# Kernel tuning notes

Measured on AMD Instinct MI355X. Metric: run time of the kernel, lower is better.

## Reference

```python
import jax, jax.numpy as jnp
import numpy as np

T, B, I, H = 512, 64, 512, 512

def setup_inputs() -> dict:
    key = jax.random.key(0)
    ks = jax.random.split(key, 16)
    s_i = 1.0 / np.sqrt(I)
    s_h = 1.0 / np.sqrt(H)
    return {
        "input": jax.random.normal(ks[0], (T, B, I), jnp.float32),
        "hidden": jax.random.normal(ks[1], (B, H), jnp.float32),
        "zt_w_w": jax.random.uniform(ks[2], (1, I), jnp.float32, -s_i, s_i),
        "zt_w_b": jax.random.uniform(ks[3], (1,), jnp.float32, -s_i, s_i),
        "zt_u_w": jax.random.uniform(ks[4], (1, H), jnp.float32, -s_h, s_h),
        "zt_u_b": jax.random.uniform(ks[5], (1,), jnp.float32, -s_h, s_h),
        "rt_w_w": jax.random.uniform(ks[6], (1, I), jnp.float32, -s_i, s_i),
        "rt_w_b": jax.random.uniform(ks[7], (1,), jnp.float32, -s_i, s_i),
        "rt_u_w": jax.random.uniform(ks[8], (1, H), jnp.float32, -s_h, s_h),
        "rt_u_b": jax.random.uniform(ks[9], (1,), jnp.float32, -s_h, s_h),
        "h_w_w": jax.random.uniform(ks[10], (H, I), jnp.float32, -s_i, s_i),
        "h_w_b": jax.random.uniform(ks[11], (H,), jnp.float32, -s_i, s_i),
        "h_u_w": jax.random.uniform(ks[12], (H, H), jnp.float32, -s_h, s_h),
        "h_u_b": jax.random.uniform(ks[13], (H,), jnp.float32, -s_h, s_h),
    }

def reference(input, hidden, zt_w_w, zt_w_b, zt_u_w, zt_u_b,
              rt_w_w, rt_w_b, rt_u_w, rt_u_b, h_w_w, h_w_b, h_u_w, h_u_b):
    # Input-dependent projections are h-independent: precompute over all T.
    xz = jnp.einsum('tbi,oi->tbo', input, zt_w_w) + zt_w_b  # [T,B,1]
    xr = jnp.einsum('tbi,oi->tbo', input, rt_w_w) + rt_w_b  # [T,B,1]
    xn = jnp.einsum('tbi,hi->tbh', input, h_w_w) + h_w_b    # [T,B,H]

    def step(h, xs):
        xz_t, xr_t, xn_t = xs
        zt = jax.nn.sigmoid(xz_t + h @ zt_u_w.T + zt_u_b)   # [B,1]
        rt = jax.nn.sigmoid(xr_t + h @ rt_u_w.T + rt_u_b)   # [B,1]
        # NOTE: faithful to source: h_u(hidden) * rt (gate applied AFTER linear)
        nt = jnp.tanh(xn_t + (h @ h_u_w.T + h_u_b) * rt)    # [B,H]
        h_new = (1.0 - zt) * nt + zt * h
        return h_new, h_new

    hidden_final, output = jax.lax.scan(step, hidden, (xz, xr, xn))
    return output, hidden_final
```

## Files before the change

### kernel.cpp

```cpp
#include <hip/hip_runtime.h>
#include <hip/hip_fp16.h>

#define T_DIM 512
#define B_DIM 64
#define I_DIM 512
#define H_DIM 512
#define BH (B_DIM * H_DIM)
#define TBH ((size_t)T_DIM * BH)

typedef __attribute__((ext_vector_type(8))) short short8;
typedef __attribute__((ext_vector_type(4))) float f32x4;

#define SW16(r, k) ((r) * 512 + ((k) ^ (((r) & 15) << 3)))

__device__ __forceinline__ unsigned short f2bf(float x) {
    unsigned int u = __float_as_uint(x);
    u = u + 0x7FFFu + ((u >> 16) & 1u);
    return (unsigned short)(u >> 16);
}
__device__ __forceinline__ float bf2f(unsigned short s) {
    return __uint_as_float(((unsigned int)s) << 16);
}
__device__ __forceinline__ float uasf(unsigned int u) { return __uint_as_float(u); }

__device__ __forceinline__ void ld128_coh(uint4& d, const void* p) {
    asm volatile("global_load_dwordx4 %0, %1, off sc0 sc1"
                 : "=v"(d) : "v"(p) : "memory");
}
__device__ __forceinline__ void ld128_coh_wait(uint4& d, const void* p) {
    asm volatile("global_load_dwordx4 %0, %1, off sc0 sc1\n\t"
                 "s_waitcnt vmcnt(0)"
                 : "=v"(d) : "v"(p) : "memory");
}
__device__ __forceinline__ void ld32f(float& d, const void* p) {
    asm volatile("global_load_dword %0, %1, off" : "=v"(d) : "v"(p));
}
__device__ __forceinline__ void ld32u(unsigned int& d, const void* p) {
    asm volatile("global_load_dword %0, %1, off" : "=v"(d) : "v"(p));
}

__global__ __launch_bounds__(256) void xzr_kernel(
    const float* __restrict__ input,
    const float* __restrict__ zw, const float* __restrict__ zb,
    const float* __restrict__ rw, const float* __restrict__ rb,
    unsigned int* __restrict__ xzr, unsigned int* __restrict__ flags)
{
    const int tid = threadIdx.x, bx = blockIdx.x;
    if (bx == 0 && tid < 32) flags[tid] = 0u;
    const int row = bx * 4 + (tid >> 6);
    const int lane = tid & 63;
    const float* p = input + (size_t)row * I_DIM + lane * 8;
    float x[8], z[8], r[8];
    *(float4*)(x)     = *(const float4*)(p);
    *(float4*)(x + 4) = *(const float4*)(p + 4);
    *(float4*)(z)     = *(const float4*)(zw + lane * 8);
    *(float4*)(z + 4) = *(const float4*)(zw + lane * 8 + 4);
    *(float4*)(r)     = *(const float4*)(rw + lane * 8);
    *(float4*)(r + 4) = *(const float4*)(rw + lane * 8 + 4);
    float pz = 0.f, pr = 0.f;
#pragma unroll
    for (int i = 0; i < 8; i++) { pz += x[i] * z[i]; pr += x[i] * r[i]; }
#pragma unroll
    for (int off = 32; off > 0; off >>= 1) {
        pz += __shfl_xor(pz, off);
        pr += __shfl_xor(pr, off);
    }
    if (lane == 0) {
        unsigned int uz = __half_as_ushort(__float2half(pz + zb[0]));
        unsigned int ur = __half_as_ushort(__float2half(pr + rb[0]));
        xzr[row] = (uz << 16) | ur;
    }
}

#define APITCH 40

__global__ __launch_bounds__(256, 2) void xn_gemm_kernel(
    const float* __restrict__ A, const float* __restrict__ W,
    const float* __restrict__ bias, float* __restrict__ C)
{
    __shared__ __align__(16) unsigned short a_hi[64 * APITCH], a_lo[64 * APITCH];
    __shared__ __align__(16) unsigned short b_hi[64 * APITCH], b_lo[64 * APITCH];
    const int tid = threadIdx.x;
    const int bx = blockIdx.x;
    const int mt = bx >> 3, ntile = bx & 7;
    const int wv = tid >> 6, lane = tid & 63;
    const int srow = tid >> 2, skseg = (tid & 3) * 8;
    const int m = lane & 15;
    const int ko = (lane >> 4) * 8;

    f32x4 ahh[4], ahl[4], alh[4];
#pragma unroll
    for (int i = 0; i < 4; i++) { ahh[i] = (f32x4)0.f; ahl[i] = (f32x4)0.f; alh[i] = (f32x4)0.f; }

    for (int kt = 0; kt < 16; ++kt) {
        {
            float fa[8], fb[8];
            const float* pa = A + (size_t)(mt * 64 + srow) * I_DIM + kt * 32 + skseg;
            *(float4*)(fa)     = *(const float4*)(pa);
            *(float4*)(fa + 4) = *(const float4*)(pa + 4);
            const float* pb = W + (size_t)(ntile * 64 + srow) * I_DIM + kt * 32 + skseg;
            *(float4*)(fb)     = *(const float4*)(pb);
            *(float4*)(fb + 4) = *(const float4*)(pb + 4);
            short8 hi, lo;
#pragma unroll
            for (int i = 0; i < 8; i++) {
                unsigned short h = f2bf(fa[i]);
                hi[i] = (short)h; lo[i] = (short)f2bf(fa[i] - bf2f(h));
            }
            *(short8*)&a_hi[srow * APITCH + skseg] = hi;
            *(short8*)&a_lo[srow * APITCH + skseg] = lo;
#pragma unroll
            for (int i = 0; i < 8; i++) {
                unsigned short h = f2bf(fb[i]);
                hi[i] = (short)h; lo[i] = (short)f2bf(fb[i] - bf2f(h));
            }
            *(short8*)&b_hi[srow * APITCH + skseg] = hi;
            *(short8*)&b_lo[srow * APITCH + skseg] = lo;
        }
        __syncthreads();
        short8 vah = *(const short8*)&a_hi[(wv * 16 + m) * APITCH + ko];
        short8 val = *(const short8*)&a_lo[(wv * 16 + m) * APITCH + ko];
#pragma unroll
        for (int ns = 0; ns < 4; ++ns) {
            short8 vbh = *(const short8*)&b_hi[(ns * 16 + m) * APITCH + ko];
            short8 vbl = *(const short8*)&b_lo[(ns * 16 + m) * APITCH + ko];
            ahh[ns] = __builtin_amdgcn_mfma_f32_16x16x32_bf16(vah, vbh, ahh[ns], 0, 0, 0);
            ahl[ns] = __builtin_amdgcn_mfma_f32_16x16x32_bf16(vah, vbl, ahl[ns], 0, 0, 0);
            alh[ns] = __builtin_amdgcn_mfma_f32_16x16x32_bf16(val, vbh, alh[ns], 0, 0, 0);
        }
        __syncthreads();
    }
#pragma unroll
    for (int ns = 0; ns < 4; ++ns) {
#pragma unroll
        for (int rr = 0; rr < 4; ++rr) {
            int rowd = wv * 16 + (lane >> 4) * 4 + rr;
            int cold = ntile * 64 + ns * 16 + (lane & 15);
            float v = ahh[ns][rr] + ahl[ns][rr] + alh[ns][rr] + bias[cold];
            C[(size_t)(mt * 64 + rowd) * H_DIM + cold] = v;
        }
    }
}

__global__ __launch_bounds__(256, 1) void rnn_kernel(
    const float* __restrict__ h0,
    const unsigned int* __restrict__ xzr,
    const float* __restrict__ zuw, const float* __restrict__ ruw,
    const float* __restrict__ zub, const float* __restrict__ rub,
    const float* __restrict__ huw, const float* __restrict__ hub,
    float* __restrict__ out,
    char* __restrict__ xbuf, unsigned int* __restrict__ flags)
{
    __shared__ __align__(16) unsigned short hs_hi[16 * 512], hs_lo[16 * 512];
    __shared__ float zu[512], ru[512];
    __shared__ float zg[16], rg[16];

    const int tid = threadIdx.x;
    const int bid = blockIdx.x;
    const int g = bid >> 3, js = bid & 7;
    const int wv = tid >> 6, lane = tid & 63;
    const int quad = lane >> 4, am = lane & 15;
    const int col = js * 64 + wv * 16 + am;
    const int ko = quad * 8;
    const int gr = tid >> 4, gs = tid & 15;

    for (int i = tid; i < 512; i += 256) { zu[i] = zuw[i]; ru[i] = ruw[i]; }
    const float zbias = zub[0], rbias = rub[0];
    const float hubl = hub[col];

    short8 wh[16], wl[16];
#pragma unroll
    for (int kt = 0; kt < 16; ++kt) {
        float f[8];
        const float* p = huw + (size_t)col * H_DIM + kt * 32 + ko;
        *(float4*)(f)     = *(const float4*)(p);
        *(float4*)(f + 4) = *(const float4*)(p + 4);
#pragma unroll
        for (int i = 0; i < 8; i++) {
            unsigned short h = f2bf(f[i]);
            wh[kt][i] = (short)h;
            wl[kt][i] = (short)f2bf(f[i] - bf2f(h));
        }
    }

#pragma unroll
    for (int i = 0; i < 8; i++) {
        int idx = tid * 4 + i * 1024;
        int row = idx >> 9, k = idx & 511;
        float4 f = *(const float4*)(h0 + (size_t)(g * 16 + row) * H_DIM + k);
        float fa[4] = {f.x, f.y, f.z, f.w};
        unsigned int h_[4], l_[4];
#pragma unroll
        for (int j = 0; j < 4; j++) {
            h_[j] = f2bf(fa[j]);
            l_[j] = f2bf(fa[j] - bf2f((unsigned short)h_[j]));
        }
        int a = SW16(row, k);
        uint2 hv = { h_[0] | (h_[1] << 16), h_[2] | (h_[3] << 16) };
        uint2 lv = { l_[0] | (l_[1] << 16), l_[2] | (l_[3] << 16) };
        *(uint2*)&hs_hi[a] = hv;
        *(uint2*)&hs_lo[a] = lv;
    }
    float hkeep[4];
#pragma unroll
    for (int rr = 0; rr < 4; ++rr)
        hkeep[rr] = h0[(size_t)(g * 16 + quad * 4 + rr) * H_DIM + col];
    __syncthreads();

    float xnv0, xnv1, xnv2, xnv3;
    unsigned int zrw;
#define PREFETCH(tt) do {                                                     \
        const float* xp_ = out + (size_t)(tt) * BH +                          \
                           (size_t)(g * 16 + quad * 4) * H_DIM + col;         \
        ld32f(xnv0, xp_);        ld32f(xnv1, xp_ + H_DIM);                    \
        ld32f(xnv2, xp_ + 2 * H_DIM); ld32f(xnv3, xp_ + 3 * H_DIM);           \
        ld32u(zrw, xzr + (tt) * B_DIM + g * 16 + gr);                         \
    } while (0)
    PREFETCH(0);

    for (int t = 0; t < T_DIM; ++t) {
        asm volatile("s_waitcnt vmcnt(0)"
                     : "+v"(xnv0), "+v"(xnv1), "+v"(xnv2), "+v"(xnv3), "+v"(zrw)
                     :: "memory");
        float pz = 0.f, pr = 0.f;
#pragma unroll
        for (int i = 0; i < 8; i++) {
            int k = gs * 4 + i * 64;
            int a = SW16(gr, k);
            uint2 hw = *(const uint2*)&hs_hi[a];
            uint2 lw = *(const uint2*)&hs_lo[a];
            float4 zv = *(const float4*)&zu[k];
            float4 rv = *(const float4*)&ru[k];
            float h0f = uasf(hw.x << 16) + uasf(lw.x << 16);
            float h1f = uasf(hw.x & 0xFFFF0000u) + uasf(lw.x & 0xFFFF0000u);
            float h2f = uasf(hw.y << 16) + uasf(lw.y << 16);
            float h3f = uasf(hw.y & 0xFFFF0000u) + uasf(lw.y & 0xFFFF0000u);
            pz += h0f * zv.x + h1f * zv.y + h2f * zv.z + h3f * zv.w;
            pr += h0f * rv.x + h1f * rv.y + h2f * rv.z + h3f * rv.w;
        }
#pragma unroll
        for (int off = 8; off > 0; off >>= 1) {
            pz += __shfl_xor(pz, off);
            pr += __shfl_xor(pr, off);
        }
        if (gs == 0) {
            float xzf = __half2float(__ushort_as_half((unsigned short)(zrw >> 16)));
            float xrf = __half2float(__ushort_as_half((unsigned short)(zrw & 0xFFFFu)));
            zg[gr] = 1.f / (1.f + __expf(-(xzf + pz + zbias)));
            rg[gr] = 1.f / (1.f + __expf(-(xrf + pr + rbias)));
        }
        __syncthreads();

        f32x4 hh = (f32x4)0.f, hl = (f32x4)0.f, lh = (f32x4)0.f;
#pragma unroll
        for (int kt = 0; kt < 16; ++kt) {
            short8 ah = *(const short8*)&hs_hi[SW16(am, kt * 32 + ko)];
            short8 al = *(const short8*)&hs_lo[SW16(am, kt * 32 + ko)];
            hh = __builtin_amdgcn_mfma_f32_16x16x32_bf16(ah, wh[kt], hh, 0, 0, 0);
            hl = __builtin_amdgcn_mfma_f32_16x16x32_bf16(ah, wl[kt], hl, 0, 0, 0);
            lh = __builtin_amdgcn_mfma_f32_16x16x32_bf16(al, wh[kt], lh, 0, 0, 0);
        }

        float xn_a[4] = {xnv0, xnv1, xnv2, xnv3};
        float* op = out + (size_t)t * BH;
        char* xb = xbuf + ((size_t)(((t & 1) * 4) + g)) * 32768;
        unsigned short* bhp = (unsigned short*)xb;
        unsigned short* blp = (unsigned short*)(xb + 16384);
#pragma unroll
        for (int rr = 0; rr < 4; ++rr) {
            int rl = quad * 4 + rr;
            float gemm = hh[rr] + hl[rr] + lh[rr] + hubl;
            float x2 = xn_a[rr] + gemm * rg[rl];
            x2 = fminf(fmaxf(x2, -30.f), 30.f);
            float e = __expf(2.f * x2);
            float ntv = (e - 1.f) / (e + 1.f);
            float hv = (1.f - zg[rl]) * ntv + zg[rl] * hkeep[rr];
            op[(size_t)(g * 16 + rl) * H_DIM + col] = hv;
            unsigned short hu = f2bf(hv);
            unsigned short lu = f2bf(hv - bf2f(hu));
            __hip_atomic_store(&bhp[rl * 512 + col], hu, __ATOMIC_RELAXED, __HIP_MEMORY_SCOPE_AGENT);
            __hip_atomic_store(&blp[rl * 512 + col], lu, __ATOMIC_RELAXED, __HIP_MEMORY_SCOPE_AGENT);
            hkeep[rr] = hv;
        }
        asm volatile("s_waitcnt vmcnt(0)" ::: "memory");
        __syncthreads();
        if (tid == 0)
            __hip_atomic_store(&flags[g * 8 + js], (unsigned int)(t + 1),
                               __ATOMIC_RELAXED, __HIP_MEMORY_SCOPE_AGENT);
        if (t == T_DIM - 1) break;

        PREFETCH(t + 1);

        if (lane < 8) {
            const unsigned int* fp = flags + g * 8 + lane;
            while (__hip_atomic_load(fp, __ATOMIC_RELAXED, __HIP_MEMORY_SCOPE_AGENT)
                   < (unsigned int)(t + 1))
                __builtin_amdgcn_s_sleep(1);
        }

        const char* src = xbuf + ((size_t)(((t & 1) * 4) + g)) * 32768 + tid * 16;
        uint4 v[8];
#pragma unroll
        for (int i = 0; i < 7; i++) ld128_coh(v[i], src + i * 4096);
        ld128_coh_wait(v[7], src + 7 * 4096);
#pragma unroll
        for (int i = 0; i < 8; i++) {
            int usidx = tid * 8 + (i & 3) * 2048;
            int row = usidx >> 9, ku = usidx & 511;
            unsigned short* dst = (i < 4) ? hs_hi : hs_lo;
            *(uint4*)&dst[SW16(row, ku)] = v[i];
        }
        __syncthreads();
    }

#pragma unroll
    for (int rr = 0; rr < 4; ++rr)
        out[TBH + (size_t)(g * 16 + quad * 4 + rr) * H_DIM + col] = hkeep[rr];
#undef PREFETCH
}

extern "C" void kernel_launch(void* const* d_in, const int* in_sizes, int n_in,
                              void* d_out, int out_size, void* d_ws, size_t ws_size,
                              hipStream_t stream)
{
    const float* input  = (const float*)d_in[0];
    const float* hidden = (const float*)d_in[1];
    const float* zt_w_w = (const float*)d_in[2];
    const float* zt_w_b = (const float*)d_in[3];
    const float* zt_u_w = (const float*)d_in[4];
    const float* zt_u_b = (const float*)d_in[5];
    const float* rt_w_w = (const float*)d_in[6];
    const float* rt_w_b = (const float*)d_in[7];
    const float* rt_u_w = (const float*)d_in[8];
    const float* rt_u_b = (const float*)d_in[9];
    const float* h_w_w  = (const float*)d_in[10];
    const float* h_w_b  = (const float*)d_in[11];
    const float* h_u_w  = (const float*)d_in[12];
    const float* h_u_b  = (const float*)d_in[13];
    float* out = (float*)d_out;

    unsigned int* flags = (unsigned int*)d_ws;
    char* xbuf = (char*)d_ws + 4096;
    unsigned int* xzr = (unsigned int*)((char*)d_ws + 4096 + 262144);

    xzr_kernel<<<dim3(8192), dim3(256), 0, stream>>>(input, zt_w_w, zt_w_b,
                                                     rt_w_w, rt_w_b, xzr, flags);
    xn_gemm_kernel<<<dim3(4096), dim3(256), 0, stream>>>(input, h_w_w, h_w_b, out);
    rnn_kernel<<<dim3(32), dim3(256), 0, stream>>>(hidden, xzr, zt_u_w, rt_u_w,
                                                   zt_u_b, rt_u_b, h_u_w, h_u_b,
                                                   out, xbuf, flags);
}
```

Baseline: 2.399 ms.

## Interleave two batch groups per block to overlap exchange latency with compute

Each recurrent block now owns two 16-row batch groups instead of one, halving the grid to 16 blocks. The two groups alternate slots, so the flag poll and coherent reload of one group's hidden state overlap the other group's gate and MFMA work. The exchanged hi/lo bf16 pair is packed into a single 32-bit word, cutting the number of atomic stores. The cost is fewer CUs doing the serial recurrence, with twice the work per block and larger shared memory and register use.

```diff
diff --git a/kernel.cpp b/kernel.cpp
--- a/kernel.cpp
+++ b/kernel.cpp
@@ -21,15 +21,9 @@
 __device__ __forceinline__ float bf2f(unsigned short s) {
     return __uint_as_float(((unsigned int)s) << 16);
 }
-__device__ __forceinline__ float uasf(unsigned int u) { return __uint_as_float(u); }
 
 __device__ __forceinline__ void ld128_coh(uint4& d, const void* p) {
     asm volatile("global_load_dwordx4 %0, %1, off sc0 sc1"
-                 : "=v"(d) : "v"(p) : "memory");
-}
-__device__ __forceinline__ void ld128_coh_wait(uint4& d, const void* p) {
-    asm volatile("global_load_dwordx4 %0, %1, off sc0 sc1\n\t"
-                 "s_waitcnt vmcnt(0)"
                  : "=v"(d) : "v"(p) : "memory");
 }
 __device__ __forceinline__ void ld32f(float& d, const void* p) {
@@ -149,20 +143,22 @@
     const float* __restrict__ zub, const float* __restrict__ rub,
     const float* __restrict__ huw, const float* __restrict__ hub,
     float* __restrict__ out,
-    char* __restrict__ xbuf, unsigned int* __restrict__ flags)
+    unsigned int* __restrict__ xbuf32, unsigned int* __restrict__ flags)
 {
-    __shared__ __align__(16) unsigned short hs_hi[16 * 512], hs_lo[16 * 512];
+    __shared__ __align__(16) unsigned short hs_hi[2][16 * 512], hs_lo[2][16 * 512];
     __shared__ float zu[512], ru[512];
-    __shared__ float zg[16], rg[16];
+    __shared__ float zg[2][16], rg[2][16];
 
     const int tid = threadIdx.x;
     const int bid = blockIdx.x;
-    const int g = bid >> 3, js = bid & 7;
+    const int js = bid & 7;
+    const int gA = (bid >> 3) * 2, gB = gA + 1;
     const int wv = tid >> 6, lane = tid & 63;
     const int quad = lane >> 4, am = lane & 15;
     const int col = js * 64 + wv * 16 + am;
     const int ko = quad * 8;
     const int gr = tid >> 4, gs = tid & 15;
+    const int lrow = tid & 15, lcolb = (tid >> 4) * 32;
 
     for (int i = tid; i < 512; i += 256) { zu[i] = zuw[i]; ru[i] = ruw[i]; }
     const float zbias = zub[0], rbias = rub[0];
@@ -184,59 +180,123 @@
     }
 
 #pragma unroll
-    for (int i = 0; i < 8; i++) {
-        int idx = tid * 4 + i * 1024;
-        int row = idx >> 9, k = idx & 511;
-        float4 f = *(const float4*)(h0 + (size_t)(g * 16 + row) * H_DIM + k);
-        float fa[4] = {f.x, f.y, f.z, f.w};
-        unsigned int h_[4], l_[4];
-#pragma unroll
-        for (int j = 0; j < 4; j++) {
-            h_[j] = f2bf(fa[j]);
-            l_[j] = f2bf(fa[j] - bf2f((unsigned short)h_[j]));
-        }
-        int a = SW16(row, k);
-        uint2 hv = { h_[0] | (h_[1] << 16), h_[2] | (h_[3] << 16) };
-        uint2 lv = { l_[0] | (l_[1] << 16), l_[2] | (l_[3] << 16) };
-        *(uint2*)&hs_hi[a] = hv;
-        *(uint2*)&hs_lo[a] = lv;
-    }
-    float hkeep[4];
-#pragma unroll
-    for (int rr = 0; rr < 4; ++rr)
-        hkeep[rr] = h0[(size_t)(g * 16 + quad * 4 + rr) * H_DIM + col];
+    for (int G = 0; G < 2; ++G) {
+        const int g = gA + G;
+        unsigned short* Hh = hs_hi[G];
+        unsigned short* Hl = hs_lo[G];
+#pragma unroll
+        for (int i = 0; i < 8; i++) {
+            int idx = tid * 4 + i * 1024;
+            int row = idx >> 9, k = idx & 511;
+            float4 f = *(const float4*)(h0 + (size_t)(g * 16 + row) * H_DIM + k);
+            float fa[4] = {f.x, f.y, f.z, f.w};
+            unsigned int h_[4], l_[4];
+#pragma unroll
+            for (int j = 0; j < 4; j++) {
+                h_[j] = f2bf(fa[j]);
+                l_[j] = f2bf(fa[j] - bf2f((unsigned short)h_[j]));
+            }
+            int a = SW16(row, k);
+            uint2 hv = { h_[0] | (h_[1] << 16), h_[2] | (h_[3] << 16) };
+            uint2 lv = { l_[0] | (l_[1] << 16), l_[2] | (l_[3] << 16) };
+            *(uint2*)&Hh[a] = hv;
+            *(uint2*)&Hl[a] = lv;
+        }
+    }
+    float hkA[4], hkB[4];
+#pragma unroll
+    for (int rr = 0; rr < 4; ++rr) {
+        hkA[rr] = h0[(size_t)(gA * 16 + quad * 4 + rr) * H_DIM + col];
+        hkB[rr] = h0[(size_t)(gB * 16 + quad * 4 + rr) * H_DIM + col];
+    }
+
+    uint4 vA[8], vB[8];
+    float xnA[4], xnB[4];
+    unsigned int zrwA = 0, zrwB = 0;
+    {
+        const float* xp = out + (size_t)(gA * 16 + quad * 4) * H_DIM + col;
+        ld32f(xnA[0], xp);             ld32f(xnA[1], xp + H_DIM);
+        ld32f(xnA[2], xp + 2 * H_DIM); ld32f(xnA[3], xp + 3 * H_DIM);
+        ld32u(zrwA, xzr + gA * 16 + gr);
+    }
     __syncthreads();
 
-    float xnv0, xnv1, xnv2, xnv3;
-    unsigned int zrw;
-#define PREFETCH(tt) do {                                                     \
-        const float* xp_ = out + (size_t)(tt) * BH +                          \
-                           (size_t)(g * 16 + quad * 4) * H_DIM + col;         \
-        ld32f(xnv0, xp_);        ld32f(xnv1, xp_ + H_DIM);                    \
-        ld32f(xnv2, xp_ + 2 * H_DIM); ld32f(xnv3, xp_ + 3 * H_DIM);           \
-        ld32u(zrw, xzr + (tt) * B_DIM + g * 16 + gr);                         \
-    } while (0)
-    PREFETCH(0);
-
-    for (int t = 0; t < T_DIM; ++t) {
+    auto slot = [&](int L, int gc, int gn, int t,
+                    bool unpack, bool issuev, bool issuex,
+                    int pollmin, int vbuf, int txn,
+                    uint4 (&vc)[8], uint4 (&vn)[8],
+                    float (&hk)[4], float (&xnc)[4], float (&xnn)[4],
+                    unsigned int& zrwc, unsigned int& zrwn)
+    {
+        unsigned short* Hh = hs_hi[L];
+        unsigned short* Hl = hs_lo[L];
+        float* zgp = zg[L];
+        float* rgp = rg[L];
+
         asm volatile("s_waitcnt vmcnt(0)"
-                     : "+v"(xnv0), "+v"(xnv1), "+v"(xnv2), "+v"(xnv3), "+v"(zrw)
+                     : "+v"(xnc[0]), "+v"(xnc[1]), "+v"(xnc[2]), "+v"(xnc[3]),
+                       "+v"(zrwc)
                      :: "memory");
+        __builtin_amdgcn_sched_barrier(0);
+
+        if (unpack) {
+#pragma unroll
+            for (int p = 0; p < 4; ++p) {
+                uint4 a = vc[2 * p], b = vc[2 * p + 1];
+                short8 h8, l8;
+                h8[0] = (short)(a.x >> 16); h8[1] = (short)(a.y >> 16);
+                h8[2] = (short)(a.z >> 16); h8[3] = (short)(a.w >> 16);
+                h8[4] = (short)(b.x >> 16); h8[5] = (short)(b.y >> 16);
+                h8[6] = (short)(b.z >> 16); h8[7] = (short)(b.w >> 16);
+                l8[0] = (short)(a.x & 0xFFFFu); l8[1] = (short)(a.y & 0xFFFFu);
+                l8[2] = (short)(a.z & 0xFFFFu); l8[3] = (short)(a.w & 0xFFFFu);
+                l8[4] = (short)(b.x & 0xFFFFu); l8[5] = (short)(b.y & 0xFFFFu);
+                l8[6] = (short)(b.z & 0xFFFFu); l8[7] = (short)(b.w & 0xFFFFu);
+                const int c = lcolb + p * 8;
+                *(short8*)&Hh[SW16(lrow, c)] = h8;
+                *(short8*)&Hl[SW16(lrow, c)] = l8;
+            }
+        }
+        __syncthreads();
+
+        if (issuev) {
+            if (lane < 8) {
+                const unsigned int* fp = flags + gn * 8 + lane;
+                while (__hip_atomic_load(fp, __ATOMIC_RELAXED,
+                                         __HIP_MEMORY_SCOPE_AGENT)
+                       < (unsigned int)pollmin)
+                    __builtin_amdgcn_s_sleep(1);
+            }
+            const char* src = (const char*)xbuf32 +
+                ((size_t)(vbuf * 4 + gn) * 8192 + lrow * 512 + lcolb) * 4;
+#pragma unroll
+            for (int i = 0; i < 8; i++) ld128_coh(vn[i], src + i * 16);
+        }
+        if (issuex) {
+            const float* xp = out + (size_t)txn * BH +
+                              (size_t)(gn * 16 + quad * 4) * H_DIM + col;
+            ld32f(xnn[0], xp);             ld32f(xnn[1], xp + H_DIM);
+            ld32f(xnn[2], xp + 2 * H_DIM); ld32f(xnn[3], xp + 3 * H_DIM);
+            ld32u(zrwn, xzr + txn * B_DIM + gn * 16 + gr);
+        }
+
         float pz = 0.f, pr = 0.f;
 #pragma unroll
-        for (int i = 0; i < 8; i++) {
-            int k = gs * 4 + i * 64;
-            int a = SW16(gr, k);
-            uint2 hw = *(const uint2*)&hs_hi[a];
-            uint2 lw = *(const uint2*)&hs_lo[a];
-            float4 zv = *(const float4*)&zu[k];
-            float4 rv = *(const float4*)&ru[k];
-            float h0f = uasf(hw.x << 16) + uasf(lw.x << 16);
-            float h1f = uasf(hw.x & 0xFFFF0000u) + uasf(lw.x & 0xFFFF0000u);
-            float h2f = uasf(hw.y << 16) + uasf(lw.y << 16);
-            float h3f = uasf(hw.y & 0xFFFF0000u) + uasf(lw.y & 0xFFFF0000u);
-            pz += h0f * zv.x + h1f * zv.y + h2f * zv.z + h3f * zv.w;
-            pr += h0f * rv.x + h1f * rv.y + h2f * rv.z + h3f * rv.w;
+        for (int i = 0; i < 4; i++) {
+            const int k = gs * 8 + i * 128;
+            const int a = SW16(gr, k);
+            short8 hw = *(const short8*)&Hh[a];
+            short8 lw = *(const short8*)&Hl[a];
+            float4 z0 = *(const float4*)&zu[k], z1 = *(const float4*)&zu[k + 4];
+            float4 r0 = *(const float4*)&ru[k], r1 = *(const float4*)&ru[k + 4];
+            float zs[8] = {z0.x, z0.y, z0.z, z0.w, z1.x, z1.y, z1.z, z1.w};
+            float rs[8] = {r0.x, r0.y, r0.z, r0.w, r1.x, r1.y, r1.z, r1.w};
+#pragma unroll
+            for (int j = 0; j < 8; j++) {
+                float hf = bf2f((unsigned short)hw[j]) + bf2f((unsigned short)lw[j]);
+                pz += hf * zs[j];
+                pr += hf * rs[j];
+            }
         }
 #pragma unroll
         for (int off = 8; off > 0; off >>= 1) {
@@ -244,79 +304,66 @@
             pr += __shfl_xor(pr, off);
         }
         if (gs == 0) {
-            float xzf = __half2float(__ushort_as_half((unsigned short)(zrw >> 16)));
-            float xrf = __half2float(__ushort_as_half((unsigned short)(zrw & 0xFFFFu)));
-            zg[gr] = 1.f / (1.f + __expf(-(xzf + pz + zbias)));
-            rg[gr] = 1.f / (1.f + __expf(-(xrf + pr + rbias)));
-        }
-        __syncthreads();
+            float xzf = __half2float(__ushort_as_half((unsigned short)(zrwc >> 16)));
+            float xrf = __half2float(__ushort_as_half((unsigned short)(zrwc & 0xFFFFu)));
+            zgp[gr] = 1.f / (1.f + __expf(-(xzf + pz + zbias)));
+            rgp[gr] = 1.f / (1.f + __expf(-(xrf + pr + rbias)));
+        }
 
         f32x4 hh = (f32x4)0.f, hl = (f32x4)0.f, lh = (f32x4)0.f;
 #pragma unroll
         for (int kt = 0; kt < 16; ++kt) {
-            short8 ah = *(const short8*)&hs_hi[SW16(am, kt * 32 + ko)];
-            short8 al = *(const short8*)&hs_lo[SW16(am, kt * 32 + ko)];
+            short8 ah = *(const short8*)&Hh[SW16(am, kt * 32 + ko)];
+            short8 al = *(const short8*)&Hl[SW16(am, kt * 32 + ko)];
             hh = __builtin_amdgcn_mfma_f32_16x16x32_bf16(ah, wh[kt], hh, 0, 0, 0);
             hl = __builtin_amdgcn_mfma_f32_16x16x32_bf16(ah, wl[kt], hl, 0, 0, 0);
             lh = __builtin_amdgcn_mfma_f32_16x16x32_bf16(al, wh[kt], lh, 0, 0, 0);
         }
-
-        float xn_a[4] = {xnv0, xnv1, xnv2, xnv3};
+        __syncthreads();
+
+        unsigned int* xb = xbuf32 + (size_t)((t & 1) * 4 + gc) * 8192;
         float* op = out + (size_t)t * BH;
-        char* xb = xbuf + ((size_t)(((t & 1) * 4) + g)) * 32768;
-        unsigned short* bhp = (unsigned short*)xb;
-        unsigned short* blp = (unsigned short*)(xb + 16384);
 #pragma unroll
         for (int rr = 0; rr < 4; ++rr) {
-            int rl = quad * 4 + rr;
+            const int rl = quad * 4 + rr;
             float gemm = hh[rr] + hl[rr] + lh[rr] + hubl;
-            float x2 = xn_a[rr] + gemm * rg[rl];
+            float x2 = xnc[rr] + gemm * rgp[rl];
             x2 = fminf(fmaxf(x2, -30.f), 30.f);
             float e = __expf(2.f * x2);
             float ntv = (e - 1.f) / (e + 1.f);
-            float hv = (1.f - zg[rl]) * ntv + zg[rl] * hkeep[rr];
-            op[(size_t)(g * 16 + rl) * H_DIM + col] = hv;
+            float hv = (1.f - zgp[rl]) * ntv + zgp[rl] * hk[rr];
+            op[(size_t)(gc * 16 + rl) * H_DIM + col] = hv;
             unsigned short hu = f2bf(hv);
             unsigned short lu = f2bf(hv - bf2f(hu));
-            __hip_atomic_store(&bhp[rl * 512 + col], hu, __ATOMIC_RELAXED, __HIP_MEMORY_SCOPE_AGENT);
-            __hip_atomic_store(&blp[rl * 512 + col], lu, __ATOMIC_RELAXED, __HIP_MEMORY_SCOPE_AGENT);
-            hkeep[rr] = hv;
+            __hip_atomic_store(&xb[rl * 512 + col],
+                               ((unsigned int)hu << 16) | (unsigned int)lu,
+                               __ATOMIC_RELAXED, __HIP_MEMORY_SCOPE_AGENT);
+            hk[rr] = hv;
         }
         asm volatile("s_waitcnt vmcnt(0)" ::: "memory");
         __syncthreads();
         if (tid == 0)
-            __hip_atomic_store(&flags[g * 8 + js], (unsigned int)(t + 1),
+            __hip_atomic_store(&flags[gc * 8 + js], (unsigned int)(t + 1),
                                __ATOMIC_RELAXED, __HIP_MEMORY_SCOPE_AGENT);
-        if (t == T_DIM - 1) break;
-
-        PREFETCH(t + 1);
-
-        if (lane < 8) {
-            const unsigned int* fp = flags + g * 8 + lane;
-            while (__hip_atomic_load(fp, __ATOMIC_RELAXED, __HIP_MEMORY_SCOPE_AGENT)
-                   < (unsigned int)(t + 1))
-                __builtin_amdgcn_s_sleep(1);
-        }
-
-        const char* src = xbuf + ((size_t)(((t & 1) * 4) + g)) * 32768 + tid * 16;
-        uint4 v[8];
-#pragma unroll
-        for (int i = 0; i < 7; i++) ld128_coh(v[i], src + i * 4096);
-        ld128_coh_wait(v[7], src + 7 * 4096);
-#pragma unroll
-        for (int i = 0; i < 8; i++) {
-            int usidx = tid * 8 + (i & 3) * 2048;
-            int row = usidx >> 9, ku = usidx & 511;
-            unsigned short* dst = (i < 4) ? hs_hi : hs_lo;
-            *(uint4*)&dst[SW16(row, ku)] = v[i];
-        }
-        __syncthreads();
-    }
-
-#pragma unroll
-    for (int rr = 0; rr < 4; ++rr)
-        out[TBH + (size_t)(g * 16 + quad * 4 + rr) * H_DIM + col] = hkeep[rr];
-#undef PREFETCH
+    };
+
+    for (int t = 0; t < T_DIM; ++t) {
+        slot(0, gA, gB, t,
+             t > 0, t > 0, true,
+             t, (t + 1) & 1, t,
+             vA, vB, hkA, xnA, xnB, zrwA, zrwB);
+        const bool nl = (t < T_DIM - 1);
+        slot(1, gB, gA, t,
+             t > 0, nl, nl,
+             t + 1, t & 1, t + 1,
+             vB, vA, hkB, xnB, xnA, zrwB, zrwA);
+    }
+
+#pragma unroll
+    for (int rr = 0; rr < 4; ++rr) {
+        out[TBH + (size_t)(gA * 16 + quad * 4 + rr) * H_DIM + col] = hkA[rr];
+        out[TBH + (size_t)(gB * 16 + quad * 4 + rr) * H_DIM + col] = hkB[rr];
+    }
 }
 
 extern "C" void kernel_launch(void* const* d_in, const int* in_sizes, int n_in,
@@ -340,13 +387,13 @@
     float* out = (float*)d_out;
 
     unsigned int* flags = (unsigned int*)d_ws;
-    char* xbuf = (char*)d_ws + 4096;
+    unsigned int* xbuf32 = (unsigned int*)((char*)d_ws + 4096);
     unsigned int* xzr = (unsigned int*)((char*)d_ws + 4096 + 262144);
 
     xzr_kernel<<<dim3(8192), dim3(256), 0, stream>>>(input, zt_w_w, zt_w_b,
                                                      rt_w_w, rt_w_b, xzr, flags);
     xn_gemm_kernel<<<dim3(4096), dim3(256), 0, stream>>>(input, h_w_w, h_w_b, out);
-    rnn_kernel<<<dim3(32), dim3(256), 0, stream>>>(hidden, xzr, zt_u_w, rt_u_w,
+    rnn_kernel<<<dim3(16), dim3(256), 0, stream>>>(hidden, xzr, zt_u_w, rt_u_w,
                                                    zt_u_b, rt_u_b, h_u_w, h_u_b,
-                                                   out, xbuf, flags);
-}
+                                                   out, xbuf32, flags);
+}
```

New measurement: 5.013 ms. +109.0%, slower.

## Compute z/r gate dot products with MFMA instead of LDS reduction

Applied to the files above, without the earlier changes.

Replaces the per-step scalar z/r gate dot-product, shuffle reduction, shared-memory broadcast and its __syncthreads with two extra MFMAs per k-tile. These use a B operand packing the hi/lo bf16 splits of zuw/ruw into columns 0-3, and the results are gathered with lane shuffles. It also moves the output store after the flag publish so the dependent blocks are signalled sooner. This removes one block barrier and LDS traffic from the serial recurrence critical path, at the cost of more MFMA work and 16 extra weight registers per lane.

```diff
diff --git a/kernel.cpp b/kernel.cpp
--- a/kernel.cpp
+++ b/kernel.cpp
@@ -21,7 +21,6 @@
 __device__ __forceinline__ float bf2f(unsigned short s) {
     return __uint_as_float(((unsigned int)s) << 16);
 }
-__device__ __forceinline__ float uasf(unsigned int u) { return __uint_as_float(u); }
 
 __device__ __forceinline__ void ld128_coh(uint4& d, const void* p) {
     asm volatile("global_load_dwordx4 %0, %1, off sc0 sc1"
@@ -152,8 +151,6 @@
     char* __restrict__ xbuf, unsigned int* __restrict__ flags)
 {
     __shared__ __align__(16) unsigned short hs_hi[16 * 512], hs_lo[16 * 512];
-    __shared__ float zu[512], ru[512];
-    __shared__ float zg[16], rg[16];
 
     const int tid = threadIdx.x;
     const int bid = blockIdx.x;
@@ -162,9 +159,7 @@
     const int quad = lane >> 4, am = lane & 15;
     const int col = js * 64 + wv * 16 + am;
     const int ko = quad * 8;
-    const int gr = tid >> 4, gs = tid & 15;
-
-    for (int i = tid; i < 512; i += 256) { zu[i] = zuw[i]; ru[i] = ruw[i]; }
+
     const float zbias = zub[0], rbias = rub[0];
     const float hubl = hub[col];
 
@@ -180,6 +175,25 @@
             unsigned short h = f2bf(f[i]);
             wh[kt][i] = (short)h;
             wl[kt][i] = (short)f2bf(f[i] - bf2f(h));
+        }
+    }
+    short8 wg[16];
+    {
+        const float* gsrc = (am & 1) ? ruw : zuw;
+#pragma unroll
+        for (int kt = 0; kt < 16; ++kt) {
+            float f[8];
+            *(float4*)(f)     = *(const float4*)(gsrc + kt * 32 + ko);
+            *(float4*)(f + 4) = *(const float4*)(gsrc + kt * 32 + ko + 4);
+            short8 v;
+#pragma unroll
+            for (int i = 0; i < 8; i++) {
+                unsigned short h = f2bf(f[i]);
+                unsigned short l = f2bf(f[i] - bf2f(h));
+                unsigned short sel = (am < 2) ? h : l;
+                v[i] = (am < 4) ? (short)sel : (short)0;
+            }
+            wg[kt] = v;
         }
     }
 
@@ -214,7 +228,7 @@
                            (size_t)(g * 16 + quad * 4) * H_DIM + col;         \
         ld32f(xnv0, xp_);        ld32f(xnv1, xp_ + H_DIM);                    \
         ld32f(xnv2, xp_ + 2 * H_DIM); ld32f(xnv3, xp_ + 3 * H_DIM);           \
-        ld32u(zrw, xzr + (tt) * B_DIM + g * 16 + gr);                         \
+        ld32u(zrw, xzr + (tt) * B_DIM + g * 16 + (lane & 15));                \
     } while (0)
     PREFETCH(0);
 
@@ -222,36 +236,10 @@
         asm volatile("s_waitcnt vmcnt(0)"
                      : "+v"(xnv0), "+v"(xnv1), "+v"(xnv2), "+v"(xnv3), "+v"(zrw)
                      :: "memory");
-        float pz = 0.f, pr = 0.f;
-#pragma unroll
-        for (int i = 0; i < 8; i++) {
-            int k = gs * 4 + i * 64;
-            int a = SW16(gr, k);
-            uint2 hw = *(const uint2*)&hs_hi[a];
-            uint2 lw = *(const uint2*)&hs_lo[a];
-            float4 zv = *(const float4*)&zu[k];
-            float4 rv = *(const float4*)&ru[k];
-            float h0f = uasf(hw.x << 16) + uasf(lw.x << 16);
-            float h1f = uasf(hw.x & 0xFFFF0000u) + uasf(lw.x & 0xFFFF0000u);
-            float h2f = uasf(hw.y << 16) + uasf(lw.y << 16);
-            float h3f = uasf(hw.y & 0xFFFF0000u) + uasf(lw.y & 0xFFFF0000u);
-            pz += h0f * zv.x + h1f * zv.y + h2f * zv.z + h3f * zv.w;
-            pr += h0f * rv.x + h1f * rv.y + h2f * rv.z + h3f * rv.w;
-        }
-#pragma unroll
-        for (int off = 8; off > 0; off >>= 1) {
-            pz += __shfl_xor(pz, off);
-            pr += __shfl_xor(pr, off);
-        }
-        if (gs == 0) {
-            float xzf = __half2float(__ushort_as_half((unsigned short)(zrw >> 16)));
-            float xrf = __half2float(__ushort_as_half((unsigned short)(zrw & 0xFFFFu)));
-            zg[gr] = 1.f / (1.f + __expf(-(xzf + pz + zbias)));
-            rg[gr] = 1.f / (1.f + __expf(-(xrf + pr + rbias)));
-        }
-        __syncthreads();
+        __builtin_amdgcn_sched_barrier(0);
 
         f32x4 hh = (f32x4)0.f, hl = (f32x4)0.f, lh = (f32x4)0.f;
+        f32x4 ga = (f32x4)0.f, gb = (f32x4)0.f;
 #pragma unroll
         for (int kt = 0; kt < 16; ++kt) {
             short8 ah = *(const short8*)&hs_hi[SW16(am, kt * 32 + ko)];
@@ -259,27 +247,42 @@
             hh = __builtin_amdgcn_mfma_f32_16x16x32_bf16(ah, wh[kt], hh, 0, 0, 0);
             hl = __builtin_amdgcn_mfma_f32_16x16x32_bf16(ah, wl[kt], hl, 0, 0, 0);
             lh = __builtin_amdgcn_mfma_f32_16x16x32_bf16(al, wh[kt], lh, 0, 0, 0);
+            ga = __builtin_amdgcn_mfma_f32_16x16x32_bf16(ah, wg[kt], ga, 0, 0, 0);
+            gb = __builtin_amdgcn_mfma_f32_16x16x32_bf16(al, wg[kt], gb, 0, 0, 0);
+        }
+
+        float zg4[4], rg4[4];
+#pragma unroll
+        for (int rr = 0; rr < 4; ++rr) {
+            float gv = ga[rr] + gb[rr];
+            float zsum = __shfl(gv, quad * 16 + 0) + __shfl(gv, quad * 16 + 2);
+            float rsum = __shfl(gv, quad * 16 + 1) + __shfl(gv, quad * 16 + 3);
+            unsigned int zw_ = (unsigned int)__shfl((int)zrw, quad * 4 + rr);
+            float xzf = __half2float(__ushort_as_half((unsigned short)(zw_ >> 16)));
+            float xrf = __half2float(__ushort_as_half((unsigned short)(zw_ & 0xFFFFu)));
+            zg4[rr] = 1.f / (1.f + __expf(-(xzf + zsum + zbias)));
+            rg4[rr] = 1.f / (1.f + __expf(-(xrf + rsum + rbias)));
         }
 
         float xn_a[4] = {xnv0, xnv1, xnv2, xnv3};
-        float* op = out + (size_t)t * BH;
         char* xb = xbuf + ((size_t)(((t & 1) * 4) + g)) * 32768;
         unsigned short* bhp = (unsigned short*)xb;
         unsigned short* blp = (unsigned short*)(xb + 16384);
+        float hva[4];
 #pragma unroll
         for (int rr = 0; rr < 4; ++rr) {
             int rl = quad * 4 + rr;
             float gemm = hh[rr] + hl[rr] + lh[rr] + hubl;
-            float x2 = xn_a[rr] + gemm * rg[rl];
+            float x2 = xn_a[rr] + gemm * rg4[rr];
             x2 = fminf(fmaxf(x2, -30.f), 30.f);
             float e = __expf(2.f * x2);
             float ntv = (e - 1.f) / (e + 1.f);
-            float hv = (1.f - zg[rl]) * ntv + zg[rl] * hkeep[rr];
-            op[(size_t)(g * 16 + rl) * H_DIM + col] = hv;
+            float hv = (1.f - zg4[rr]) * ntv + zg4[rr] * hkeep[rr];
             unsigned short hu = f2bf(hv);
             unsigned short lu = f2bf(hv - bf2f(hu));
             __hip_atomic_store(&bhp[rl * 512 + col], hu, __ATOMIC_RELAXED, __HIP_MEMORY_SCOPE_AGENT);
             __hip_atomic_store(&blp[rl * 512 + col], lu, __ATOMIC_RELAXED, __HIP_MEMORY_SCOPE_AGENT);
+            hva[rr] = hv;
             hkeep[rr] = hv;
         }
         asm volatile("s_waitcnt vmcnt(0)" ::: "memory");
@@ -287,6 +290,13 @@
         if (tid == 0)
             __hip_atomic_store(&flags[g * 8 + js], (unsigned int)(t + 1),
                                __ATOMIC_RELAXED, __HIP_MEMORY_SCOPE_AGENT);
+
+        {
+            float* op = out + (size_t)t * BH;
+#pragma unroll
+            for (int rr = 0; rr < 4; ++rr)
+                op[(size_t)(g * 16 + quad * 4 + rr) * H_DIM + col] = hva[rr];
+        }
         if (t == T_DIM - 1) break;
 
         PREFETCH(t + 1);
```

After: 2.382 ms. No clear change (-0.7%).
